# Kernel optimization log

Hardware: AMD Instinct MI355X
Metric: run time of the kernel (lower is better)

Reference implementation:

```python
import jax, jax.numpy as jnp
import numpy as np

D_MODEL = 1024
N_HEADS = 16
HEAD_DIM = D_MODEL // N_HEADS
D_FF = 4 * D_MODEL
EPS = 1e-5


def layer_norm(x, gamma, beta):
    mu = jnp.mean(x, axis=-1, keepdims=True)
    var = jnp.var(x, axis=-1, keepdims=True)
    return (x - mu) * jax.lax.rsqrt(var + EPS) * gamma + beta


def setup_inputs() -> dict:
    key = jax.random.key(0)
    ks = jax.random.split(key, 12)
    B, T, S = 4, 2048, 2048
    s_in = 1.0 / np.sqrt(D_MODEL)
    s_ff = 1.0 / np.sqrt(D_FF)
    return {
        "x": jax.random.normal(ks[0], (B, T, D_MODEL), jnp.float32),
        "context": jax.random.normal(ks[1], (B, S, D_MODEL), jnp.float32),
        "Wq": jax.random.normal(ks[2], (D_MODEL, D_MODEL), jnp.float32) * s_in,
        "Wk": jax.random.normal(ks[3], (D_MODEL, D_MODEL), jnp.float32) * s_in,
        "Wv": jax.random.normal(ks[4], (D_MODEL, D_MODEL), jnp.float32) * s_in,
        "Wo": jax.random.normal(ks[5], (D_MODEL, D_MODEL), jnp.float32) * s_in,
        "W1": jax.random.normal(ks[6], (D_FF, D_MODEL), jnp.float32) * s_in,
        "W2": jax.random.normal(ks[7], (D_MODEL, D_FF), jnp.float32) * s_ff,
        "g1": jnp.ones((D_MODEL,), jnp.float32),
        "b1": jnp.zeros((D_MODEL,), jnp.float32),
        "gc": jnp.ones((D_MODEL,), jnp.float32),
        "bc": jnp.zeros((D_MODEL,), jnp.float32),
        "g2": jnp.ones((D_MODEL,), jnp.float32),
        "b2": jnp.zeros((D_MODEL,), jnp.float32),
    }


def reference(x, context, Wq, Wk, Wv, Wo, W1, W2, g1, b1, gc, bc, g2, b2):
    B, T, C = x.shape
    S = context.shape[1]
    residual = x
    xn = layer_norm(x, g1, b1)
    cn = layer_norm(context, gc, bc)
    # torch Linear: y = x @ W.T ; split heads -> [B, H, T, Dh]
    q = (xn @ Wq.T).reshape(B, T, N_HEADS, HEAD_DIM).transpose(0, 2, 1, 3)
    k = (cn @ Wk.T).reshape(B, S, N_HEADS, HEAD_DIM).transpose(0, 2, 1, 3)
    v = (cn @ Wv.T).reshape(B, S, N_HEADS, HEAD_DIM).transpose(0, 2, 1, 3)
    scale = HEAD_DIM ** (-0.5)
    attn = jax.nn.softmax(jnp.einsum('bhtd,bhsd->bhts', q, k) * scale, axis=-1)
    o = jnp.einsum('bhts,bhsd->bhtd', attn, v).transpose(0, 2, 1, 3).reshape(B, T, C)
    x = residual + o @ Wo.T
    residual = x
    h = layer_norm(x, g2, b2)
    h = jax.nn.gelu(h @ W1.T, approximate=False) @ W2.T
    return residual + h
```

## Files before the change

### kernel.cpp

```cpp
#include <hip/hip_runtime.h>
#include <cstdint>
#include <cstddef>

typedef __attribute__((ext_vector_type(8))) short short8;
typedef __attribute__((ext_vector_type(4))) short short4v;
typedef __attribute__((ext_vector_type(4))) float f32x4;
typedef __attribute__((ext_vector_type(2))) unsigned uint2v;

#define DEV static __device__ __forceinline__

DEV short f2bf(float f) {
    unsigned u = __builtin_bit_cast(unsigned, f);
    unsigned r = (u + 0x7fffu + ((u >> 16) & 1u)) >> 16;
    return (short)r;
}

DEV unsigned cvt_pk_bf16(float a, float b) {
    unsigned r;
    asm("v_cvt_pk_bf16_f32 %0, %1, %2" : "=v"(r) : "v"(a), "v"(b));
    return r;
}

DEV float exp2_hw(float x) {
    float r;
    asm("v_exp_f32 %0, %1" : "=v"(r) : "v"(x));
    return r;
}

DEV void gld16(const void* g, void* l) {
    __builtin_amdgcn_global_load_lds((const __attribute__((address_space(1))) void*)g,
                                     (__attribute__((address_space(3))) void*)l, 16, 0, 0);
}

#define MFMA(c, a, b) asm volatile("v_mfma_f32_16x16x32_bf16 %0, %1, %2, %0" : "+v"(c) : "v"(a), "v"(b))
#define BAR() asm volatile("s_barrier" ::: "memory")

__global__ __launch_bounds__(256) void cvt_weights(
    const float* __restrict__ wq, const float* __restrict__ wk,
    const float* __restrict__ wv, const float* __restrict__ wo,
    const float* __restrict__ w1, const float* __restrict__ w2,
    short* __restrict__ dst) {
    long long gid = (long long)blockIdx.x * 256 + threadIdx.x;
    long long i4 = gid * 4;
    const float* src; long long loc;
    if (i4 < (4LL << 20)) {
        int s = (int)(i4 >> 20);
        src = (s == 0) ? wq : (s == 1) ? wk : (s == 2) ? wv : wo;
        loc = i4 & ((1LL << 20) - 1);
    } else {
        long long r = i4 - (4LL << 20);
        int s = (int)(r >> 22);
        src = s ? w2 : w1;
        loc = r & ((1LL << 22) - 1);
    }
    float4 v = *(const float4*)(src + loc);
    short4v o;
    o.x = f2bf(v.x); o.y = f2bf(v.y); o.z = f2bf(v.z); o.w = f2bf(v.w);
    *(short4v*)(dst + i4) = o;
}

__global__ __launch_bounds__(256) void ln_bf16(const float* __restrict__ x,
                                               const float* __restrict__ g,
                                               const float* __restrict__ bt,
                                               short* __restrict__ out) {
    int row = blockIdx.x;
    const float4* xr = (const float4*)(x + (size_t)row * 1024);
    float4 v = xr[threadIdx.x];
    float s  = v.x + v.y + v.z + v.w;
    float s2 = v.x*v.x + v.y*v.y + v.z*v.z + v.w*v.w;
    #pragma unroll
    for (int m = 1; m < 64; m <<= 1) { s += __shfl_xor(s, m); s2 += __shfl_xor(s2, m); }
    __shared__ float red[8];
    int wid = threadIdx.x >> 6;
    if ((threadIdx.x & 63) == 0) { red[wid] = s; red[4 + wid] = s2; }
    __syncthreads();
    s  = red[0] + red[1] + red[2] + red[3];
    s2 = red[4] + red[5] + red[6] + red[7];
    float mu  = s * (1.0f / 1024.0f);
    float var = fmaxf(s2 * (1.0f / 1024.0f) - mu * mu, 0.0f);
    float rs  = rsqrtf(var + 1e-5f);
    float4 gv = ((const float4*)g)[threadIdx.x];
    float4 bv = ((const float4*)bt)[threadIdx.x];
    short4v o;
    o.x = f2bf((v.x - mu) * rs * gv.x + bv.x);
    o.y = f2bf((v.y - mu) * rs * gv.y + bv.y);
    o.z = f2bf((v.z - mu) * rs * gv.z + bv.z);
    o.w = f2bf((v.w - mu) * rs * gv.w + bv.w);
    *(short4v*)(out + (size_t)row * 1024 + (size_t)threadIdx.x * 4) = o;
}

template<int MODE>
DEV void gemm_core(const short* __restrict__ A, const short* __restrict__ B,
                   void* __restrict__ out, const float* __restrict__ resid,
                   int N, int K, int lda, int ldb, float osc, int bm, int bn) {
    __shared__ short lds[2 * 32768];
    const int tid = threadIdx.x;
    const int row0 = bm << 8, col0 = bn << 8;
    const int wid = tid >> 6, lane = tid & 63;
    const int wm = wid >> 2, wn = wid & 3;
    const int lr = lane & 15, lg = lane >> 4;
    const int NK = K >> 6;

    auto stage = [&](int kt, int which) {
        int d = kt & 1;
        const short* src; int rb; int ld;
        if (which < 2) { src = A; rb = row0; ld = lda; } else { src = B; rb = col0; ld = ldb; }
        int rhalf = (which & 1) << 7;
        short* dst = lds + d * 32768 + which * 8192;
        #pragma unroll
        for (int l = 0; l < 2; ++l) {
            int g = l * 512 + tid;
            int r = g >> 3, c = g & 7;
            gld16(src + (size_t)(rb + rhalf + r) * ld + kt * 64 + ((c ^ (r & 7)) << 3),
                  dst + g * 8);
        }
    };

    f32x4 acc[8][4] = {};

    stage(0, 0); stage(0, 1); stage(0, 2); stage(0, 3);
    if (NK > 1) {
        stage(1, 2); stage(1, 3);
        asm volatile("s_waitcnt vmcnt(4)" ::: "memory");
    } else {
        asm volatile("s_waitcnt vmcnt(0)" ::: "memory");
    }
    BAR();

    const int rBbase = (wn & 1) << 6;
    for (int t = 0; t < NK; ++t) {
        const short* bufA = lds + (t & 1) * 32768 + wm * 8192;
        const short* bufB = lds + (t & 1) * 32768 + 16384 + (wn >> 1) * 8192;
        bool st1 = (t + 1) < NK, st2 = (t + 2) < NK;
        short8 bf2[2][4];

        {
            short8 af[4];
            #pragma unroll
            for (int i = 0; i < 4; ++i) {
                int r = i * 16 + lr;
                af[i] = *(const short8*)(bufA + r * 64 + ((lg ^ (r & 7)) << 3));
            }
            #pragma unroll
            for (int j = 0; j < 4; ++j) {
                int rB = rBbase + j * 16 + lr;
                bf2[0][j] = *(const short8*)(bufB + rB * 64 + ((lg ^ (rB & 7)) << 3));
            }
            if (st1) stage(t + 1, 0);
            BAR();
            __builtin_amdgcn_s_setprio(1);
            #pragma unroll
            for (int i = 0; i < 4; ++i)
                #pragma unroll
                for (int j = 0; j < 4; ++j)
                    MFMA(acc[i][j], af[i], bf2[0][j]);
            __builtin_amdgcn_s_setprio(0);
            BAR();
        }
        {
            short8 af[4];
            #pragma unroll
            for (int i = 0; i < 4; ++i) {
                int r = i * 16 + lr;
                af[i] = *(const short8*)(bufA + r * 64 + (((4 + lg) ^ (r & 7)) << 3));
            }
            #pragma unroll
            for (int j = 0; j < 4; ++j) {
                int rB = rBbase + j * 16 + lr;
                bf2[1][j] = *(const short8*)(bufB + rB * 64 + (((4 + lg) ^ (rB & 7)) << 3));
            }
            if (st1) stage(t + 1, 1);
            BAR();
            __builtin_amdgcn_s_setprio(1);
            #pragma unroll
            for (int i = 0; i < 4; ++i)
                #pragma unroll
                for (int j = 0; j < 4; ++j)
                    MFMA(acc[i][j], af[i], bf2[1][j]);
            __builtin_amdgcn_s_setprio(0);
            BAR();
        }
        {
            short8 af[4];
            #pragma unroll
            for (int i = 0; i < 4; ++i) {
                int r = 64 + i * 16 + lr;
                af[i] = *(const short8*)(bufA + r * 64 + ((lg ^ (r & 7)) << 3));
            }
            if (st2) stage(t + 2, 2);
            BAR();
            __builtin_amdgcn_s_setprio(1);
            #pragma unroll
            for (int i = 0; i < 4; ++i)
                #pragma unroll
                for (int j = 0; j < 4; ++j)
                    MFMA(acc[4 + i][j], af[i], bf2[0][j]);
            __builtin_amdgcn_s_setprio(0);
            BAR();
        }
        {
            short8 af[4];
            #pragma unroll
            for (int i = 0; i < 4; ++i) {
                int r = 64 + i * 16 + lr;
                af[i] = *(const short8*)(bufA + r * 64 + (((4 + lg) ^ (r & 7)) << 3));
            }
            if (st2) stage(t + 2, 3);
            BAR();
            __builtin_amdgcn_s_setprio(1);
            #pragma unroll
            for (int i = 0; i < 4; ++i)
                #pragma unroll
                for (int j = 0; j < 4; ++j)
                    MFMA(acc[4 + i][j], af[i], bf2[1][j]);
            __builtin_amdgcn_s_setprio(0);
            if (st2)      asm volatile("s_waitcnt vmcnt(4)" ::: "memory");
            else if (st1) asm volatile("s_waitcnt vmcnt(0)" ::: "memory");
            BAR();
        }
    }
    asm volatile("s_nop 7\n\ts_nop 7");

    int orow0 = row0 + wm * 128, ocol0 = col0 + wn * 64;
    #pragma unroll
    for (int i = 0; i < 8; ++i)
        #pragma unroll
        for (int j = 0; j < 4; ++j)
            #pragma unroll
            for (int r = 0; r < 4; ++r) {
                int gr = orow0 + i * 16 + lg * 4 + r;
                int gc = ocol0 + j * 16 + lr;
                size_t off = (size_t)gr * N + gc;
                float v = acc[i][j][r];
                if constexpr (MODE == 1) {
                    ((float*)out)[off] = resid ? v + resid[off] : v;
                } else if constexpr (MODE == 2) {
                    float tg = 0.5f * v * (1.0f + erff(v * 0.70710678118f));
                    ((short*)out)[off] = f2bf(tg);
                } else {
                    ((short*)out)[off] = f2bf(v * osc);
                }
            }
}

__global__ __launch_bounds__(512, 2) void gemm_qkv(
    const short* __restrict__ XN, const short* __restrict__ CN,
    const short* __restrict__ Wq, const short* __restrict__ Wk, const short* __restrict__ Wv,
    short* __restrict__ QB, short* __restrict__ KB, short* __restrict__ VT, float qscale) {
    int sid = (blockIdx.x & 7) * 48 + (blockIdx.x >> 3);
    int sub = sid >> 7, i = sid & 127;
    const short *A, *B; short* o; float osc; int N, bm, bn;
    if (sub == 0)      { A = XN; B = Wq; o = QB; osc = qscale; N = 1024; bm = i >> 2; bn = i & 3; }
    else if (sub == 1) { A = CN; B = Wk; o = KB; osc = 1.0f;   N = 1024; bm = i >> 2; bn = i & 3; }
    else               { A = Wv; B = CN; o = VT; osc = 1.0f;   N = 8192; bm = i >> 5; bn = i & 31; }
    gemm_core<3>(A, B, o, nullptr, N, 1024, 1024, 1024, osc, bm, bn);
}

template<int MODE>
__global__ __launch_bounds__(512, 2) void gemm_std(const short* __restrict__ A,
                                                   const short* __restrict__ B,
                                                   void* __restrict__ out,
                                                   const float* __restrict__ resid,
                                                   int N, int K, float osc) {
    int cpx = gridDim.x >> 3;
    int sid = (blockIdx.x & 7) * cpx + (blockIdx.x >> 3);
    int nbn = N >> 8;
    int bm = sid / nbn, bn = sid % nbn;
    gemm_core<MODE>(A, B, out, resid, N, K, K, K, osc, bm, bn);
}

__global__ __launch_bounds__(512, 2) void gemm_ff2(const short* __restrict__ F1,
                                                   const short* __restrict__ W2,
                                                   float* __restrict__ dOut,
                                                   float* __restrict__ P2,
                                                   const float* __restrict__ X2) {
    int sid = (blockIdx.x & 7) * 32 + (blockIdx.x >> 3);
    int h = sid >> 7, i = sid & 127;
    int bm = i >> 2, bn = i & 3;
    const short* A = F1 + h * 2048;
    const short* B = W2 + h * 2048;
    float* o = h ? P2 : dOut;
    const float* r = h ? nullptr : X2;
    gemm_core<1>(A, B, o, r, 1024, 2048, 4096, 4096, 1.0f, bm, bn);
}

__global__ __launch_bounds__(256) void add_f32(float* __restrict__ dst,
                                               const float* __restrict__ src, int n4) {
    int i = blockIdx.x * 256 + threadIdx.x;
    int stride = gridDim.x * 256;
    for (; i < n4; i += stride) {
        float4 a = ((const float4*)dst)[i];
        float4 b = ((const float4*)src)[i];
        a.x += b.x; a.y += b.y; a.z += b.z; a.w += b.w;
        ((float4*)dst)[i] = a;
    }
}

__global__ __launch_bounds__(256) void attn(const short* __restrict__ Q,
                                            const short* __restrict__ K,
                                            const short* __restrict__ Vt,
                                            short* __restrict__ O) {
    __shared__ short lK[64 * 64];
    __shared__ short lV[64 * 64];
    __shared__ short lP[4][32 * 64];
    int tid = threadIdx.x;
    int qt = blockIdx.x & 15;
    int bh = blockIdx.x >> 4;
    int b = bh >> 4, h = bh & 15;
    int wid = tid >> 6, lane = tid & 63;
    int lr = lane & 15, lg = lane >> 4;
    int q0 = qt * 128 + wid * 32;

    short8 qf[2][2];
    #pragma unroll
    for (int fm = 0; fm < 2; ++fm)
        #pragma unroll
        for (int kb = 0; kb < 2; ++kb) {
            size_t roff = (size_t)(b * 2048 + q0 + fm * 16 + lr) * 1024 + h * 64 + kb * 32 + lg * 8;
            qf[fm][kb] = *(const short8*)(Q + roff);
        }

    f32x4 oacc[2][4] = {};
    float mrow[2] = { -1e30f, -1e30f };
    float lrs[2]  = { 0.0f, 0.0f };

    const short* Kb = K + (size_t)(b * 2048) * 1024 + h * 64;
    const short* Vb = Vt + (size_t)(h * 64) * 8192 + b * 2048;
    short* Pw = lP[wid];
    int albase = (lane & 48) >> 2;

    for (int st = 0; st < 32; ++st) {
        #pragma unroll
        for (int c = 0; c < 2; ++c) {
            int idx = c * 256 + tid;
            int r = idx >> 3, sp = idx & 7;
            int sl = sp ^ (r & 7);
            gld16(Kb + (size_t)(st * 64 + r) * 1024 + sl * 8, &lK[idx * 8]);
            gld16(Vb + (size_t)r * 8192 + st * 64 + sl * 8, &lV[idx * 8]);
        }
        __syncthreads();

        f32x4 sc2[4][2] = {};
        #pragma unroll
        for (int kb = 0; kb < 2; ++kb) {
            short8 kf[4];
            #pragma unroll
            for (int fn = 0; fn < 4; ++fn) {
                int kr = fn * 16 + lr;
                kf[fn] = *(const short8*)(lK + kr * 64 + (((kb * 4 + lg) ^ (kr & 7)) << 3));
            }
            #pragma unroll
            for (int fn = 0; fn < 4; ++fn)
                #pragma unroll
                for (int fm = 0; fm < 2; ++fm)
                    MFMA(sc2[fn][fm], kf[fn], qf[fm][kb]);
        }
        asm volatile("s_nop 7\n\ts_nop 7");

        #pragma unroll
        for (int fm = 0; fm < 2; ++fm) {
            float pm = sc2[0][fm][0];
            #pragma unroll
            for (int fn = 0; fn < 4; ++fn)
                #pragma unroll
                for (int r = 0; r < 4; ++r)
                    if (fn | r) pm = fmaxf(pm, sc2[fn][fm][r]);
            pm = fmaxf(pm, __shfl_xor(pm, 16));
            pm = fmaxf(pm, __shfl_xor(pm, 32));

            float mo = mrow[fm];
            float mn = mo;
            float al = 1.0f;
            if (!__all(pm <= mo + 8.0f)) {
                mn = fmaxf(mo, pm);
                al = exp2_hw(mo - mn);
                mrow[fm] = mn;
                #pragma unroll
                for (int r = 0; r < 4; ++r) {
                    float alr = __shfl(al, albase + r);
                    #pragma unroll
                    for (int fn = 0; fn < 4; ++fn) oacc[fm][fn][r] *= alr;
                }
            }

            float p[4][4];
            float ps = 0.0f;
            #pragma unroll
            for (int fn = 0; fn < 4; ++fn)
                #pragma unroll
                for (int r = 0; r < 4; ++r) {
                    p[fn][r] = exp2_hw(sc2[fn][fm][r] - mn);
                    ps += p[fn][r];
                }
            ps += __shfl_xor(ps, 16);
            ps += __shfl_xor(ps, 32);
            lrs[fm] = lrs[fm] * al + ps;

            int pr = fm * 16 + lr;
            int swz = (pr & 7) << 3;
            #pragma unroll
            for (int fn = 0; fn < 4; ++fn) {
                uint2v w;
                w.x = cvt_pk_bf16(p[fn][0], p[fn][1]);
                w.y = cvt_pk_bf16(p[fn][2], p[fn][3]);
                *(uint2v*)(Pw + ((pr * 64 + fn * 16 + lg * 4) ^ swz)) = w;
            }
        }

        #pragma unroll
        for (int kb = 0; kb < 2; ++kb) {
            short8 pa[2], vf[4];
            #pragma unroll
            for (int fm = 0; fm < 2; ++fm) {
                int pr = fm * 16 + lr;
                pa[fm] = *(const short8*)(Pw + pr * 64 + (((kb * 4 + lg) ^ (pr & 7)) << 3));
            }
            #pragma unroll
            for (int fn = 0; fn < 4; ++fn) {
                int vr = fn * 16 + lr;
                vf[fn] = *(const short8*)(lV + vr * 64 + (((kb * 4 + lg) ^ (vr & 7)) << 3));
            }
            #pragma unroll
            for (int fm = 0; fm < 2; ++fm)
                #pragma unroll
                for (int fn = 0; fn < 4; ++fn)
                    MFMA(oacc[fm][fn], pa[fm], vf[fn]);
        }
        __syncthreads();
    }
    asm volatile("s_nop 7\n\ts_nop 7");

    #pragma unroll
    for (int fm = 0; fm < 2; ++fm)
        #pragma unroll
        for (int r = 0; r < 4; ++r) {
            float linv = __shfl(lrs[fm], albase + r);
            float inv = 1.0f / linv;
            #pragma unroll
            for (int fn = 0; fn < 4; ++fn) {
                size_t off = (size_t)(b * 2048 + q0 + fm * 16 + lg * 4 + r) * 1024 + h * 64 + fn * 16 + lr;
                O[off] = f2bf(oacc[fm][fn][r] * inv);
            }
        }
}

extern "C" void kernel_launch(void* const* d_in, const int* in_sizes, int n_in,
                              void* d_out, int out_size, void* d_ws, size_t ws_size,
                              hipStream_t stream) {
    const float* x   = (const float*)d_in[0];
    const float* ctx = (const float*)d_in[1];
    const float* Wq  = (const float*)d_in[2];
    const float* Wk  = (const float*)d_in[3];
    const float* Wv  = (const float*)d_in[4];
    const float* Wo  = (const float*)d_in[5];
    const float* W1  = (const float*)d_in[6];
    const float* W2  = (const float*)d_in[7];
    const float* g1  = (const float*)d_in[8];
    const float* b1  = (const float*)d_in[9];
    const float* gc  = (const float*)d_in[10];
    const float* bc  = (const float*)d_in[11];
    const float* g2  = (const float*)d_in[12];
    const float* b2  = (const float*)d_in[13];

    char* ws = (char*)d_ws;
    const size_t OFF_W  = 0;
    const size_t OFF_XN = 25165824;
    const size_t OFF_CN = OFF_XN + 16777216;
    const size_t OFF_QB = OFF_CN + 16777216;
    const size_t OFF_KB = OFF_QB + 16777216;
    const size_t OFF_VT = OFF_KB + 16777216;
    const size_t OFF_X2 = OFF_VT + 16777216;
    const size_t OFF_F1 = OFF_X2 + 33554432;

    short* Wb = (short*)(ws + OFF_W);
    short* XN = (short*)(ws + OFF_XN);
    short* CN = (short*)(ws + OFF_CN);
    short* QB = (short*)(ws + OFF_QB);
    short* KB = (short*)(ws + OFF_KB);
    short* VT = (short*)(ws + OFF_VT);
    float* X2 = (float*)(ws + OFF_X2);
    short* F1 = (short*)(ws + OFF_F1);
    short* OB = XN;
    short* H  = CN;
    float* P2 = (float*)(ws + OFF_QB);

    const size_t WQo = 0, WKo = 1048576, WVo = 2097152, WOo = 3145728;
    const size_t W1o = 4194304, W2o = 8388608;
    const float QSCALE = 0.125f * 1.4426950408889634f;

    cvt_weights<<<12288, 256, 0, stream>>>(Wq, Wk, Wv, Wo, W1, W2, Wb);
    ln_bf16<<<8192, 256, 0, stream>>>(x, g1, b1, XN);
    ln_bf16<<<8192, 256, 0, stream>>>(ctx, gc, bc, CN);
    gemm_qkv<<<384, 512, 0, stream>>>(XN, CN, Wb + WQo, Wb + WKo, Wb + WVo, QB, KB, VT, QSCALE);
    attn<<<1024, 256, 0, stream>>>(QB, KB, VT, OB);
    gemm_std<1><<<128, 512, 0, stream>>>(OB, Wb + WOo, X2, x, 1024, 1024, 1.0f);
    ln_bf16<<<8192, 256, 0, stream>>>(X2, g2, b2, H);
    gemm_std<2><<<512, 512, 0, stream>>>(H, Wb + W1o, F1, nullptr, 4096, 1024, 1.0f);
    gemm_ff2<<<256, 512, 0, stream>>>(F1, Wb + W2o, (float*)d_out, P2, X2);
    add_f32<<<2048, 256, 0, stream>>>((float*)d_out, P2, 2097152);
}
```

Baseline: 490.4 us.

## Double-buffer attention K/V tiles, widen blocks to 512 threads, use tanh GELU

The attention kernel now uses 8 waves per block covering 256 query rows and double-buffers the K/V LDS tiles, so the next tile's global-to-LDS loads overlap with the current tile's MFMA work. Block indices are also remapped so blocks are interleaved across XCDs. In the FF1 epilogue, exact erf GELU is replaced by a tanh-style approximation built from hardware exp2 and rcp. That approximation changes numerics slightly, and the larger blocks raise LDS use per block.

```diff
diff --git a/kernel.cpp b/kernel.cpp
--- a/kernel.cpp
+++ b/kernel.cpp
@@ -25,6 +25,18 @@
     float r;
     asm("v_exp_f32 %0, %1" : "=v"(r) : "v"(x));
     return r;
+}
+
+DEV float rcp_hw(float x) {
+    float r;
+    asm("v_rcp_f32 %0, %1" : "=v"(r) : "v"(x));
+    return r;
+}
+
+DEV float gelu_f(float v) {
+    float t  = v * (1.0f + 0.044715f * v * v);
+    float e  = exp2_hw(fminf(2.3022082f * t, 126.0f));
+    return v * e * rcp_hw(e + 1.0f);
 }
 
 DEV void gld16(const void* g, void* l) {
@@ -235,8 +247,7 @@
                 if constexpr (MODE == 1) {
                     ((float*)out)[off] = resid ? v + resid[off] : v;
                 } else if constexpr (MODE == 2) {
-                    float tg = 0.5f * v * (1.0f + erff(v * 0.70710678118f));
-                    ((short*)out)[off] = f2bf(tg);
+                    ((short*)out)[off] = f2bf(gelu_f(v));
                 } else {
                     ((short*)out)[off] = f2bf(v * osc);
                 }
@@ -296,20 +307,20 @@
     }
 }
 
-__global__ __launch_bounds__(256) void attn(const short* __restrict__ Q,
+__global__ __launch_bounds__(512) void attn(const short* __restrict__ Q,
                                             const short* __restrict__ K,
                                             const short* __restrict__ Vt,
                                             short* __restrict__ O) {
-    __shared__ short lK[64 * 64];
-    __shared__ short lV[64 * 64];
-    __shared__ short lP[4][32 * 64];
+    __shared__ short lK[2][64 * 64];
+    __shared__ short lV[2][64 * 64];
+    __shared__ short lP[8][32 * 64];
     int tid = threadIdx.x;
-    int qt = blockIdx.x & 15;
-    int bh = blockIdx.x >> 4;
+    int sid = (blockIdx.x & 7) * 64 + (blockIdx.x >> 3);
+    int bh = sid >> 3, qt = sid & 7;
     int b = bh >> 4, h = bh & 15;
     int wid = tid >> 6, lane = tid & 63;
     int lr = lane & 15, lg = lane >> 4;
-    int q0 = qt * 128 + wid * 32;
+    int q0 = qt * 256 + wid * 32;
 
     short8 qf[2][2];
     #pragma unroll
@@ -329,16 +340,20 @@
     short* Pw = lP[wid];
     int albase = (lane & 48) >> 2;
 
+    int sr = tid >> 3, sc = tid & 7;
+    int ssl = sc ^ (sr & 7);
+    auto stage = [&](int st, int d) {
+        gld16(Kb + (size_t)(st * 64 + sr) * 1024 + ssl * 8, &lK[d][tid * 8]);
+        gld16(Vb + (size_t)sr * 8192 + st * 64 + ssl * 8, &lV[d][tid * 8]);
+    };
+
+    stage(0, 0);
+    asm volatile("s_waitcnt vmcnt(0)" ::: "memory");
+    BAR();
+
     for (int st = 0; st < 32; ++st) {
-        #pragma unroll
-        for (int c = 0; c < 2; ++c) {
-            int idx = c * 256 + tid;
-            int r = idx >> 3, sp = idx & 7;
-            int sl = sp ^ (r & 7);
-            gld16(Kb + (size_t)(st * 64 + r) * 1024 + sl * 8, &lK[idx * 8]);
-            gld16(Vb + (size_t)r * 8192 + st * 64 + sl * 8, &lV[idx * 8]);
-        }
-        __syncthreads();
+        int d = st & 1;
+        if (st + 1 < 32) stage(st + 1, d ^ 1);
 
         f32x4 sc2[4][2] = {};
         #pragma unroll
@@ -347,7 +362,7 @@
             #pragma unroll
             for (int fn = 0; fn < 4; ++fn) {
                 int kr = fn * 16 + lr;
-                kf[fn] = *(const short8*)(lK + kr * 64 + (((kb * 4 + lg) ^ (kr & 7)) << 3));
+                kf[fn] = *(const short8*)(lK[d] + kr * 64 + (((kb * 4 + lg) ^ (kr & 7)) << 3));
             }
             #pragma unroll
             for (int fn = 0; fn < 4; ++fn)
@@ -418,7 +433,7 @@
             #pragma unroll
             for (int fn = 0; fn < 4; ++fn) {
                 int vr = fn * 16 + lr;
-                vf[fn] = *(const short8*)(lV + vr * 64 + (((kb * 4 + lg) ^ (vr & 7)) << 3));
+                vf[fn] = *(const short8*)(lV[d] + vr * 64 + (((kb * 4 + lg) ^ (vr & 7)) << 3));
             }
             #pragma unroll
             for (int fm = 0; fm < 2; ++fm)
@@ -426,7 +441,9 @@
                 for (int fn = 0; fn < 4; ++fn)
                     MFMA(oacc[fm][fn], pa[fm], vf[fn]);
         }
-        __syncthreads();
+
+        asm volatile("s_waitcnt vmcnt(0)" ::: "memory");
+        BAR();
     }
     asm volatile("s_nop 7\n\ts_nop 7");
 
@@ -492,7 +509,7 @@
     ln_bf16<<<8192, 256, 0, stream>>>(x, g1, b1, XN);
     ln_bf16<<<8192, 256, 0, stream>>>(ctx, gc, bc, CN);
     gemm_qkv<<<384, 512, 0, stream>>>(XN, CN, Wb + WQo, Wb + WKo, Wb + WVo, QB, KB, VT, QSCALE);
-    attn<<<1024, 256, 0, stream>>>(QB, KB, VT, OB);
+    attn<<<512, 512, 0, stream>>>(QB, KB, VT, OB);
     gemm_std<1><<<128, 512, 0, stream>>>(OB, Wb + WOo, X2, x, 1024, 1024, 1.0f);
     ln_bf16<<<8192, 256, 0, stream>>>(X2, g2, b2, H);
     gemm_std<2><<<512, 512, 0, stream>>>(H, Wb + W1o, F1, nullptr, 4096, 1024, 1.0f);
```

Measured after the change: 469.1 us. 1.05x faster.
